# Kernel optimization log

Measured on AMD Instinct MI355X. Metric: run time of the kernel, lower is better.

The kernel has to match this reference:

```python
import jax, jax.numpy as jnp
import numpy as np

B, T1, O, E, H = 32, 65, 384, 384, 768  # T1 = T+1


def setup_inputs() -> dict:
    key = jax.random.key(0)
    ks = jax.random.split(key, 10)
    s = 0.05
    return {
        "target": jax.random.randint(ks[0], (B, T1), 0, O),
        "hidden": jax.random.normal(ks[1], (B, H), jnp.float32),
        "teacher_forcing_ratio": 1,
        "emb_table": jax.random.normal(ks[2], (O, E), jnp.float32) * s,
        "attn_W": jax.random.normal(ks[3], (H, H + O), jnp.float32) * s,
        "attn_b": jnp.zeros((H,), jnp.float32),
        "v_W": jax.random.normal(ks[4], (1, H), jnp.float32) * s,
        "gru_Wih": jax.random.normal(ks[5], (3 * H, E + O), jnp.float32) * s,
        "gru_Whh": jax.random.normal(ks[6], (3 * H, H), jnp.float32) * s,
        "gru_bih": jnp.zeros((3 * H,), jnp.float32),
        "gru_bhh": jnp.zeros((3 * H,), jnp.float32),
        "fc_W": jax.random.normal(ks[7], (O, E + O + H), jnp.float32) * s,
        "fc_b": jnp.zeros((O,), jnp.float32),
    }


def reference(target, hidden, teacher_forcing_ratio, emb_table, attn_W, attn_b,
              v_W, gru_Wih, gru_Whh, gru_bih, gru_bhh, fc_W, fc_b):
    # teacher_forcing_ratio == 1: always teacher-forced (deterministic)
    Bt, T1_ = target.shape
    T = T1_ - 1
    Od = fc_b.shape[0]
    Hd = hidden.shape[1]
    pos = jnp.arange(T1_)
    hist0 = jnp.zeros((Bt, T1_, Od), hidden.dtype)  # slot 0 = initial zeros output

    def step(carry, xs):
        h, hist = carry
        i, tok = xs
        emb = emb_table[tok]  # (B, E)
        # Bahdanau attention over history positions 0..i
        hrep = jnp.broadcast_to(h[:, None, :], (Bt, T1_, Hd))
        energy = jnp.tanh(jnp.concatenate([hrep, hist], -1) @ attn_W.T + attn_b)
        scores = jnp.squeeze(energy @ v_W.T, -1)  # (B, T1)
        scores = jnp.where(pos <= i, scores, -jnp.inf)
        a = jax.nn.softmax(scores, axis=-1)
        w = jnp.einsum('bt,bto->bo', a, hist)  # context (B, O)
        # single-step GRU (PyTorch gate order r, z, n)
        x = jnp.concatenate([emb, w], -1)
        gi = x @ gru_Wih.T + gru_bih
        gh = h @ gru_Whh.T + gru_bhh
        ir, iz, inn = jnp.split(gi, 3, axis=-1)
        hr, hz, hn = jnp.split(gh, 3, axis=-1)
        r = jax.nn.sigmoid(ir + hr)
        z = jax.nn.sigmoid(iz + hz)
        n = jnp.tanh(inn + r * hn)
        h_new = (1.0 - z) * n + z * h
        out = jnp.concatenate([h_new, w, emb], -1) @ fc_W.T + fc_b  # (B, O)
        hist = hist.at[:, i + 1].set(out)
        return (h_new, hist), (out, a)

    xs = (jnp.arange(T), target[:, :T].T)  # input token at step i is target[:, i]
    _, (outs, attns) = jax.lax.scan(step, (hidden, hist0), xs)
    outputs = jnp.transpose(outs, (1, 2, 0))  # (B, O, T)
    # flatten per-step attentions: step i has i+1 valid entries -> T*(T+1)/2 total
    rows = np.concatenate([np.full(i + 1, i) for i in range(T)])
    cols = np.concatenate([np.arange(i + 1) for i in range(T)])
    attentions = attns[rows, :, cols].T  # (B, T*(T+1)/2)
    return outputs, attentions
```

## Files before the change

kernel.cpp:

```cpp
#include <hip/hip_runtime.h>


#define DEVI static __device__ __forceinline__
typedef float f32x4 __attribute__((ext_vector_type(4)));
typedef unsigned u32x4 __attribute__((ext_vector_type(4)));
typedef unsigned u32x2 __attribute__((ext_vector_type(2)));
typedef unsigned short ushort_t;

constexpr int ATTN_OFF = 786432;

constexpr int OFF_HALL  = 0;
constexpr int OFF_U     = 1597440;
constexpr int OFF_WALL  = 1622016;
constexpr int OFF_HISTF = 2408448;
constexpr int OFF_GH    = 3194880;
constexpr int OFF_GIE   = 3268608;
constexpr int OFF_FE    = 3342336;
constexpr int OFF_GE    = 3354624;
constexpr int OFF_FP    = 3379200;
constexpr int OFF_CP    = 3391488;
constexpr int OFF_GHM   = 3416064;
constexpr int OFF_GWM   = 4005888;
constexpr int OFF_GEM   = 4300800;
constexpr int OFF_GB    = 4595712;
constexpr int OFF_V1    = 4596480;
constexpr int OFF_BAR   = 4596512;
constexpr int OFF_F32END= 4597664;
constexpr int O16_CALL = 0;
constexpr int O16_HIST = 1572864;

DEVI float fast_tanh(float x) {
  float a = __builtin_fabsf(x);
  float e = __expf(-2.0f * a);
  float r = __fdividef(1.0f - e, 1.0f + e);
  return __builtin_copysignf(r, x);
}
DEVI float sigmoidf_(float x) { return __fdividef(1.0f, 1.0f + __expf(-x)); }
DEVI float bflo(unsigned u) { return __uint_as_float(u << 16); }
DEVI float bfhi(unsigned u) { return __uint_as_float(u & 0xffff0000u); }
DEVI unsigned f2bf(float f) {
  unsigned u = __float_as_uint(f);
  return (u + 0x7fffu + ((u >> 16) & 1u)) >> 16;
}

DEVI float nc_ld_f1(const float* p) {
  float r;
  asm volatile("global_load_dword %0, %1, off sc0 sc1\n\ts_waitcnt vmcnt(0)"
               : "=&v"(r) : "v"(p) : "memory");
  return r;
}
DEVI f32x4 nc_ld4(const float* p) {
  f32x4 r;
  asm volatile("global_load_dwordx4 %0, %1, off sc0 sc1\n\ts_waitcnt vmcnt(0)"
               : "=&v"(r) : "v"(p) : "memory");
  return r;
}
DEVI void nc_ld4x2(const float* p0, const float* p1, f32x4& r0, f32x4& r1) {
  asm volatile(
      "global_load_dwordx4 %0, %2, off sc0 sc1\n\t"
      "global_load_dwordx4 %1, %3, off sc0 sc1\n\t"
      "s_waitcnt vmcnt(0)"
      : "=&v"(r0), "=&v"(r1) : "v"(p0), "v"(p1) : "memory");
}
DEVI void nc_st4(float* p, f32x4 v) {
  asm volatile("global_store_dwordx4 %0, %1, off sc0 sc1" :: "v"(p), "v"(v) : "memory");
}
DEVI void nc_st2u(ushort_t* p, u32x2 v) {
  asm volatile("global_store_dwordx2 %0, %1, off sc0 sc1" :: "v"(p), "v"(v) : "memory");
}
DEVI void nc_st_f1(float* p, float v_) {
  asm volatile("global_store_dword %0, %1, off sc0 sc1" :: "v"(p), "v"(v_) : "memory");
}

DEVI void gridbar(unsigned* bar) {
  asm volatile("s_waitcnt vmcnt(0)" ::: "memory");
  __syncthreads();
  if (threadIdx.x == 0) {
    unsigned* super = bar + 1024;
    unsigned* gen   = bar + 1056;
    unsigned g = __hip_atomic_load(gen, __ATOMIC_RELAXED, __HIP_MEMORY_SCOPE_AGENT);
    int grp = (int)(blockIdx.x >> 3);
    unsigned a = __hip_atomic_fetch_add(bar + grp * 32, 1u, __ATOMIC_RELAXED, __HIP_MEMORY_SCOPE_AGENT);
    bool released = false;
    if (a == 7u) {
      __hip_atomic_store(bar + grp * 32, 0u, __ATOMIC_RELAXED, __HIP_MEMORY_SCOPE_AGENT);
      unsigned s = __hip_atomic_fetch_add(super, 1u, __ATOMIC_RELAXED, __HIP_MEMORY_SCOPE_AGENT);
      if (s == 31u) {
        __hip_atomic_store(super, 0u, __ATOMIC_RELAXED, __HIP_MEMORY_SCOPE_AGENT);
        __hip_atomic_fetch_add(gen, 1u, __ATOMIC_RELAXED, __HIP_MEMORY_SCOPE_AGENT);
        released = true;
      }
    }
    if (!released) {
      while (__hip_atomic_load(gen, __ATOMIC_RELAXED, __HIP_MEMORY_SCOPE_AGENT) == g) {
        __builtin_amdgcn_s_sleep(1);
      }
    }
  }
  __syncthreads();
}

__global__ __launch_bounds__(256) void kprepG(const float* __restrict__ attn_W,
                                              const float* __restrict__ fcW,
                                              const float* __restrict__ fcb,
                                              float* __restrict__ ws) {
  int bid = blockIdx.x, tid = threadIdx.x;
  if (bid < 288) {
    int rt = bid / 6, kt = bid % 6;
    int r0 = rt * 16;
    int kg = kt * 256 + tid;
    float acc[16];
#pragma unroll
    for (int q = 0; q < 16; ++q) acc[q] = 0.f;
    for (int o = 0; o < 384; ++o) {
      float f = fcW[o * 1536 + kg];
#pragma unroll
      for (int q = 0; q < 16; ++q)
        acc[q] = fmaf(attn_W[(r0 + q) * 1152 + 768 + o], f, acc[q]);
    }
#pragma unroll
    for (int q = 0; q < 16; ++q) {
      int r = r0 + q;
      if (kg < 768)       ws[OFF_GHM + r * 768 + kg] = acc[q];
      else if (kg < 1152) ws[OFF_GWM + r * 384 + (kg - 768)] = acc[q];
      else                ws[OFF_GEM + r * 384 + (kg - 1152)] = acc[q];
    }
  } else {
    for (int r = tid; r < 768; r += 256) {
      float a = 0.f;
      for (int o = 0; o < 384; ++o) a = fmaf(attn_W[r * 1152 + 768 + o], fcb[o], a);
      ws[OFF_GB + r] = a;
    }
  }
}

__global__ __launch_bounds__(256) void kprep0(const float* __restrict__ hidden,
                                              const float* __restrict__ vW,
                                              float* __restrict__ ws) {
  ushort_t* w16 = (ushort_t*)(ws + OFF_F32END);
  int bid = blockIdx.x, tid = threadIdx.x;
  int gtid = bid * 256 + tid;
  if (gtid < 24576) {
    int k = gtid >> 5, b = gtid & 31;
    ws[OFF_HALL + gtid] = hidden[b * 768 + k];
  } else if (gtid < 36864) {
    ((unsigned*)(w16 + O16_CALL))[gtid - 24576] = 0u;
  } else if (gtid < 43008) {
    ((unsigned*)(w16 + O16_HIST))[gtid - 36864] = 0u;
  }
  if (gtid < 1152) ((unsigned*)(ws + OFF_BAR))[gtid] = 0u;
  if (bid == 0) {
    __shared__ float vred[256];
    float a = 0.f;
    for (int k = tid; k < 768; k += 256) a += __builtin_fabsf(vW[k]);
    vred[tid] = a;
    __syncthreads();
    for (int s2 = 128; s2 > 0; s2 >>= 1) {
      if (tid < s2) vred[tid] += vred[tid + s2];
      __syncthreads();
    }
    if (tid == 0) ws[OFF_V1] = vred[0];
  }
}

__global__ void __launch_bounds__(1024)
kmain(const int* __restrict__ target, const float* __restrict__ emb,
      const float* __restrict__ attn_W, const float* __restrict__ attn_b,
      const float* __restrict__ vW,
      const float* __restrict__ Wih, const float* __restrict__ Whh,
      const float* __restrict__ bih, const float* __restrict__ bhh,
      const float* __restrict__ fcW, const float* __restrict__ fcb,
      float* __restrict__ outp, float* __restrict__ ws) {
  const int bid = blockIdx.x, tid = threadIdx.x;
  const int wv = tid >> 6, lane = tid & 63;
  const int b32 = lane & 31, kh = lane >> 5;
  const int vb = ((bid & 7) << 5) | (bid >> 3);
  const int xcd = vb >> 5, slot = vb & 31;
  unsigned* bar = (unsigned*)(ws + OFF_BAR);
  ushort_t* w16 = (ushort_t*)(ws + OFF_F32END);

  __shared__ __align__(16) float sW_A[8 * 768];
  __shared__ __align__(16) float sW_B[16 * 384];
  __shared__ __align__(16) float sW_GH[12 * 768];
  __shared__ __align__(16) float sW_C[14 * 384];
  __shared__ __align__(16) float sUn[13536];

  const int gbA = (vb * 480) >> 8, geA = ((vb + 1) * 480) >> 8;
  const int rbA = gbA * 4;
  const int nswA = geA - gbA;
  const int nRA = nswA * 4;
  const int lb  = xcd * 28 + (slot - 4);
  const int rbB = (slot >= 4) ? (lb * 3456) / 224 : 0;
  const int reB = (slot >= 4) ? ((lb + 1) * 3456) / 224 : 0;
  const int nB  = reB - rbB;
  const int gbG = (slot >= 4) ? (lb * 576) / 224 : 0;
  const int geG = (slot >= 4) ? ((lb + 1) * 576) / 224 : 0;
  const int nswG = geG - gbG;
  const int nRG = nswG * 4;
  const int rbC = xcd * 144 + ((slot * 144) >> 5);
  const int reC = xcd * 144 + (((slot + 1) * 144) >> 5);

  for (int lr = 0; lr < nRA; ++lr) {
    int row = rbA + lr;
    const float* src;
    if (row < 768)       src = attn_W + row * 1152;
    else if (row < 1536) src = ws + OFF_GHM + (row - 768) * 768;
    else                 src = fcW + (row - 1536) * 1536;
    if (tid < 768) sW_A[lr * 768 + tid] = src[tid];
  }
  if (slot >= 4) {
    for (int lr = 0; lr < nB; ++lr) {
      int row = rbB + lr;
      const float* src;
      if (row < 2304)      src = Wih + row * 768;
      else if (row < 2688) src = fcW + (row - 2304) * 1536 + 1152;
      else                 src = ws + OFF_GEM + (row - 2688) * 384;
      if (tid < 384) sW_B[lr * 384 + tid] = src[tid];
    }
    for (int lr = 0; lr < nRG; ++lr) {
      int row = gbG * 4 + lr;
      if (tid < 768) sW_GH[lr * 768 + tid] = Whh[row * 768 + tid];
    }
  }
  for (int lr = 0; lr < 14; ++lr) {
    const float* src = nullptr;
    if (lr < 9) {
      int grow = vb * 3 + (lr / 3) + (lr % 3) * 768;
      src = Wih + grow * 768 + 384;
    } else {
      int r = rbC + (lr - 9);
      if (r < reC) src = (r < 384) ? fcW + r * 1536 + 768
                                   : ws + OFF_GWM + (r - 384) * 384;
    }
    if (src && tid < 384) sW_C[lr * 384 + tid] = src[tid];
  }
  __syncthreads();

  const float Mv = ws[OFF_V1];
  const int k0 = wv * 48 + kh * 24;

  for (int i = 0; i < 64; ++i) {
    {
      float* part_  = sUn;
      float* stage  = sUn + 4096;
      float* stage2 = sUn + 4352;
      float xr[24];
      const float* hb = ws + OFF_HALL + i * 24576 + b32;
#pragma unroll
      for (int q = 0; q < 24; ++q) xr[q] = hb[(k0 + q) * 32];

      float a[8];
#pragma unroll
      for (int r = 0; r < 8; ++r) a[r] = 0.f;
#pragma unroll
      for (int r = 0; r < 8; ++r) {
        if (r < nRA) {
          int row = rbA + r;
          if (!(i == 0 && row >= 768)) {
            const float* wp = &sW_A[r * 768 + k0];
            float acc = 0.f;
#pragma unroll
            for (int q = 0; q < 6; ++q) {
              f32x4 w = *(const f32x4*)(wp + q * 4);
              acc = fmaf(w[0], xr[q * 4 + 0], acc);
              acc = fmaf(w[1], xr[q * 4 + 1], acc);
              acc = fmaf(w[2], xr[q * 4 + 2], acc);
              acc = fmaf(w[3], xr[q * 4 + 3], acc);
            }
            a[r] = acc;
          }
        }
      }
#pragma unroll
      for (int r = 0; r < 8; ++r) a[r] += __shfl_xor(a[r], 32);
      if (kh == 0) {
#pragma unroll
        for (int r = 0; r < 8; ++r) part_[wv * 256 + r * 32 + b32] = a[r];
      }
      __syncthreads();
      if (tid < 256) {
        int rr = tid >> 5, bb = tid & 31;
        float sum = 0.f;
#pragma unroll
        for (int w2 = 0; w2 < 16; ++w2) sum += part_[w2 * 256 + tid];
        if (rr < nRA) {
          int row = rbA + rr;
          if (row < 768) sum += attn_b[row];
          stage[rr * 32 + bb] = sum;
        }
      } else if (tid < 320) {
        int t2 = tid - 256, rr = t2 >> 3, bq = t2 & 7;
        if (rr < nRA && i > 0) {
          int row = rbA + rr;
          if (row >= 768) {
            const float* src = row < 1536
                ? ws + OFF_CP + (row - 768) * 32 + bq * 4
                : ws + OFF_FP + (row - 1536) * 32 + bq * 4;
            *(f32x4*)&stage2[rr * 32 + bq * 4] = nc_ld4(src);
          }
        }
      }
      __syncthreads();
      if (tid < 64) {
        int gsel = tid >> 5, sub = tid & 31;
        if (gsel < nswA) {
          int row0 = rbA + gsel * 4;
          int e0 = gsel * 4;
          if (row0 < 768) {
            f32x4 v = {stage[e0 * 32 + sub], stage[(e0 + 1) * 32 + sub],
                       stage[(e0 + 2) * 32 + sub], stage[(e0 + 3) * 32 + sub]};
            nc_st4(ws + OFF_U + sub * 768 + row0, v);
          } else if (i > 0) {
            float v0 = stage[e0 * 32 + sub] + stage2[e0 * 32 + sub];
            float v1 = stage[(e0 + 1) * 32 + sub] + stage2[(e0 + 1) * 32 + sub];
            float v2 = stage[(e0 + 2) * 32 + sub] + stage2[(e0 + 2) * 32 + sub];
            float v3 = stage[(e0 + 3) * 32 + sub] + stage2[(e0 + 3) * 32 + sub];
            u32x2 pk;
            pk[0] = f2bf(v0) | (f2bf(v1) << 16);
            pk[1] = f2bf(v2) | (f2bf(v3) << 16);
            if (row0 < 1536) {
              nc_st2u(w16 + O16_CALL + i * 24576 + sub * 768 + (row0 - 768), pk);
            } else {
              nc_st2u(w16 + O16_HIST + i * 12288 + sub * 384 + (row0 - 1536), pk);
              f32x4 vf = {v0, v1, v2, v3};
              nc_st4(ws + OFF_HISTF + i * 12288 + sub * 384 + (row0 - 1536), vf);
            }
          }
        }
      }
    }
    gridbar(bar);

    if (slot < 4) {
      const int bb = xcd * 4 + (vb & 3);
      float* u_s   = sUn;
      float* p_l   = sUn + 768;
      float* d_l   = sUn + 832;
      float* wred2 = sUn + 848;
      if (tid < 192) *(f32x4*)&u_s[tid * 4] = nc_ld4(ws + OFF_U + bb * 768 + tid * 4);
      if (tid < 64) p_l[tid] = 0.f;
      __syncthreads();
      const int tl = tid >> 5, kc = tid & 31;
      float u_r[24], v_r[24];
#pragma unroll
      for (int q = 0; q < 24; ++q) {
        u_r[q] = u_s[kc * 24 + q];
        v_r[q] = vW[kc * 24 + q];
      }
#pragma unroll
      for (int rr2 = 0; rr2 < 2; ++rr2) {
        int t = rr2 * 32 + tl;
        float s = 0.f;
        if (t <= i) {
          const ushort_t* cb = w16 + O16_CALL + t * 24576 + bb * 768 + kc * 24;
          u32x4 c0 = ((const u32x4*)cb)[0];
          u32x4 c1 = ((const u32x4*)cb)[1];
          u32x4 c2 = ((const u32x4*)cb)[2];
#pragma unroll
          for (int j = 0; j < 4; ++j) {
            s = fmaf(fast_tanh(u_r[2 * j] + bflo(c0[j])), v_r[2 * j], s);
            s = fmaf(fast_tanh(u_r[2 * j + 1] + bfhi(c0[j])), v_r[2 * j + 1], s);
            s = fmaf(fast_tanh(u_r[8 + 2 * j] + bflo(c1[j])), v_r[8 + 2 * j], s);
            s = fmaf(fast_tanh(u_r[8 + 2 * j + 1] + bfhi(c1[j])), v_r[8 + 2 * j + 1], s);
            s = fmaf(fast_tanh(u_r[16 + 2 * j] + bflo(c2[j])), v_r[16 + 2 * j], s);
            s = fmaf(fast_tanh(u_r[16 + 2 * j + 1] + bfhi(c2[j])), v_r[16 + 2 * j + 1], s);
          }
        }
#pragma unroll
        for (int d2 = 16; d2 >= 1; d2 >>= 1) s += __shfl_xor(s, d2);
        if (kc == 0 && t <= i) p_l[t] = __expf(s - Mv);
      }
      __syncthreads();
      if (tid < 64) {
        float pv = p_l[tid];
#pragma unroll
        for (int d = 1; d < 64; d <<= 1) pv += __shfl_xor(pv, d);
        if (tid == 0) d_l[0] = __fdividef(1.0f, pv);
      }
      __syncthreads();
      float dinv = d_l[0];
      if (tid >= 768 && tid < 832) {
        int t = tid - 768;
        if (t <= i)
          outp[ATTN_OFF + bb * 2080 + (i * (i + 1)) / 2 + t] = p_l[t] * dinv;
      }
      if (tid < 768) {
        int opair = tid % 192, tpar = tid / 192;
        int o0 = opair * 2;
        const ushort_t* hbase = w16 + O16_HIST + bb * 384 + o0;
        float a0 = 0.f, a1 = 0.f;
        int t = tpar;
        for (; t + 4 <= i; t += 8) {
          unsigned hv0 = *(const unsigned*)(hbase + t * 12288);
          unsigned hv1 = *(const unsigned*)(hbase + (t + 4) * 12288);
          float p0 = p_l[t], p1 = p_l[t + 4];
          a0 = fmaf(p0, bflo(hv0), a0);
          a1 = fmaf(p0, bfhi(hv0), a1);
          a0 = fmaf(p1, bflo(hv1), a0);
          a1 = fmaf(p1, bfhi(hv1), a1);
        }
        if (t <= i) {
          unsigned hv = *(const unsigned*)(hbase + t * 12288);
          float p = p_l[t];
          a0 = fmaf(p, bflo(hv), a0);
          a1 = fmaf(p, bfhi(hv), a1);
        }
        wred2[tpar * 384 + o0]     = a0;
        wred2[tpar * 384 + o0 + 1] = a1;
      }
      __syncthreads();
      if (tid < 96) {
        f32x4 v;
#pragma unroll
        for (int e = 0; e < 4; ++e) {
          int o = tid * 4 + e;
          v[e] = (wred2[o] + wred2[384 + o] + wred2[768 + o] + wred2[1152 + o]) * dinv;
        }
        nc_st4(ws + OFF_WALL + i * 12288 + bb * 384 + tid * 4, v);
      }
    } else {
      float* part_  = sUn;
      float* stageB = sUn + 2048;
      float* ghst   = sUn + 8192;
      const int gl = wv >> 2, kq = wv & 3;
      const int tok = target[b32 * 65 + i];
      const int koff = kq * 96 + kh * 48;
      const float* xe = emb + tok * 384 + koff;
      f32x4 x_[12];
#pragma unroll
      for (int q = 0; q < 12; ++q) x_[q] = *(const f32x4*)(xe + q * 4);
      float a[4];
#pragma unroll
      for (int r = 0; r < 4; ++r) {
        int lr = gl * 4 + r;
        float acc = 0.f;
        if (lr < nB) {
          const float* wp = &sW_B[lr * 384 + koff];
#pragma unroll
          for (int q = 0; q < 12; ++q) {
            f32x4 w = *(const f32x4*)(wp + q * 4);
            acc = fmaf(w[0], x_[q][0], acc);
            acc = fmaf(w[1], x_[q][1], acc);
            acc = fmaf(w[2], x_[q][2], acc);
            acc = fmaf(w[3], x_[q][3], acc);
          }
        }
        a[r] = acc;
      }
#pragma unroll
      for (int r = 0; r < 4; ++r) a[r] += __shfl_xor(a[r], 32);
      if (kh == 0) {
#pragma unroll
        for (int r = 0; r < 4; ++r)
          part_[((gl * 4 + r) * 4 + kq) * 32 + b32] = a[r];
      }
      __syncthreads();
      if (tid < 512) {
        int glr = tid >> 5, bb = tid & 31;
        if (glr < nB) {
          float sum = part_[(glr * 4 + 0) * 32 + bb] + part_[(glr * 4 + 1) * 32 + bb]
                    + part_[(glr * 4 + 2) * 32 + bb] + part_[(glr * 4 + 3) * 32 + bb];
          int row = rbB + glr;
          if (row < 2304) sum += bih[row];
          else if (row < 2688) sum += fcb[row - 2304];
          else sum += ws[OFF_GB + (row - 2688)];
          stageB[glr * 32 + bb] = sum;
        }
      }
      __syncthreads();
      if (tid < 128) {
        int r16 = tid >> 3, bq = tid & 7;
        if (r16 < nB) {
          int row = rbB + r16;
          f32x4 v = *(f32x4*)&stageB[r16 * 32 + bq * 4];
          float* dst;
          if (row < 2304) dst = ws + OFF_GIE + row * 32 + bq * 4;
          else if (row < 2688) dst = ws + OFF_FE + (row - 2304) * 32 + bq * 4;
          else dst = ws + OFF_GE + (row - 2688) * 32 + bq * 4;
          nc_st4(dst, v);
        }
      }
      __syncthreads();
      {
        float xr2[24];
        const float* hb2 = ws + OFF_HALL + i * 24576 + b32;
#pragma unroll
        for (int q = 0; q < 24; ++q) xr2[q] = hb2[(k0 + q) * 32];
        float a2[12];
#pragma unroll
        for (int r = 0; r < 12; ++r) a2[r] = 0.f;
#pragma unroll
        for (int r = 0; r < 12; ++r) {
          if (r < nRG) {
            const float* wp = &sW_GH[r * 768 + k0];
            float acc = 0.f;
#pragma unroll
            for (int q = 0; q < 6; ++q) {
              f32x4 w = *(const f32x4*)(wp + q * 4);
              acc = fmaf(w[0], xr2[q * 4 + 0], acc);
              acc = fmaf(w[1], xr2[q * 4 + 1], acc);
              acc = fmaf(w[2], xr2[q * 4 + 2], acc);
              acc = fmaf(w[3], xr2[q * 4 + 3], acc);
            }
            a2[r] = acc;
          }
        }
#pragma unroll
        for (int r = 0; r < 12; ++r) a2[r] += __shfl_xor(a2[r], 32);
        if (kh == 0) {
#pragma unroll
          for (int r = 0; r < 12; ++r) part_[wv * 384 + r * 32 + b32] = a2[r];
        }
        __syncthreads();
        if (tid < 384) {
          int rr = tid >> 5, bb = tid & 31;
          if (rr < nRG) {
            float sum = 0.f;
#pragma unroll
            for (int w2 = 0; w2 < 16; ++w2) sum += part_[w2 * 384 + tid];
            ghst[rr * 32 + bb] = sum + bhh[gbG * 4 + rr];
          }
        }
        __syncthreads();
        if (tid < 96) {
          int rr = tid >> 3, bq = tid & 7;
          if (rr < nRG)
            nc_st4(ws + OFF_GH + (gbG * 4 + rr) * 32 + bq * 4,
                   *(f32x4*)&ghst[rr * 32 + bq * 4]);
        }
      }
    }
    gridbar(bar);

    {
      float* w_lds   = sUn;
      float* g_lds   = sUn + 12416;
      float* giw_lds = sUn + 12992;
      float* fpst    = sUn + 13280;
      float* gat     = sUn + 13440;
      {
        int b = tid >> 5, c = tid & 31;
        const float* src = ws + OFF_WALL + i * 12288 + tid * 12;
        float* dst = w_lds + b * 388 + c * 12;
        *(f32x4*)&dst[0] = *(const f32x4*)(src);
        *(f32x4*)&dst[4] = *(const f32x4*)(src + 4);
        *(f32x4*)&dst[8] = *(const f32x4*)(src + 8);
      }
      __syncthreads();
      if (wv < 9) {
        int jl = wv / 3, gg = wv % 3;
        const float* wp = &sW_C[(jl * 3 + gg) * 384 + kh * 192];
        const float* xp = w_lds + b32 * 388 + kh * 192;
        float acc = 0.f;
#pragma unroll 8
        for (int q = 0; q < 48; ++q) {
          f32x4 wq4 = *(const f32x4*)(wp + q * 4);
          f32x4 xq4 = *(const f32x4*)(xp + q * 4);
          acc = fmaf(wq4[0], xq4[0], acc); acc = fmaf(wq4[1], xq4[1], acc);
          acc = fmaf(wq4[2], xq4[2], acc); acc = fmaf(wq4[3], xq4[3], acc);
        }
        acc += __shfl_xor(acc, 32);
        if (kh == 0) giw_lds[(jl * 3 + gg) * 32 + b32] = acc;
      } else if (wv < 14) {
        int r = rbC + (wv - 9);
        if (r < reC) {
          const float* wp = &sW_C[(9 + (wv - 9)) * 384 + kh * 192];
          const float* xp = w_lds + b32 * 388 + kh * 192;
          float acc = 0.f;
#pragma unroll 8
          for (int q = 0; q < 48; ++q) {
            f32x4 wq4 = *(const f32x4*)(wp + q * 4);
            f32x4 xq4 = *(const f32x4*)(xp + q * 4);
            acc = fmaf(wq4[0], xq4[0], acc); acc = fmaf(wq4[1], xq4[1], acc);
            acc = fmaf(wq4[2], xq4[2], acc); acc = fmaf(wq4[3], xq4[3], acc);
          }
          acc += __shfl_xor(acc, 32);
          if (kh == 0) fpst[(wv - 9) * 32 + b32] = acc;
        }
      } else {
        int t2 = tid - 896;
        if (t2 < 72) {
          int q0 = 2 * t2, q1 = 2 * t2 + 1;
          const float* pa;
          const float* pb;
          {
            int row = q0 >> 3, bq = q0 & 7;
            int rr2 = row < 9 ? row : row - 9;
            int r = vb * 3 + (rr2 % 3) + (rr2 / 3) * 768;
            pa = ws + (row < 9 ? OFF_GIE : OFF_GH) + r * 32 + bq * 4;
          }
          {
            int row = q1 >> 3, bq = q1 & 7;
            int rr2 = row < 9 ? row : row - 9;
            int r = vb * 3 + (rr2 % 3) + (rr2 / 3) * 768;
            pb = ws + (row < 9 ? OFF_GIE : OFF_GH) + r * 32 + bq * 4;
          }
          f32x4 v0, v1;
          nc_ld4x2(pa, pb, v0, v1);
          *(f32x4*)&g_lds[q0 * 4] = v0;
          *(f32x4*)&g_lds[q1 * 4] = v1;
        }
      }
      __syncthreads();
      if (tid < 96) {
        int jl = tid >> 5, bb = tid & 31;
        int j = vb * 3 + jl;
        float gi_r = g_lds[jl * 32 + bb];
        float gi_z = g_lds[(3 + jl) * 32 + bb];
        float gi_n = g_lds[(6 + jl) * 32 + bb];
        float gh_r = g_lds[(9 + jl) * 32 + bb];
        float gh_z = g_lds[(12 + jl) * 32 + bb];
        float gh_n = g_lds[(15 + jl) * 32 + bb];
        float giw_r = giw_lds[(jl * 3 + 0) * 32 + bb];
        float giw_z = giw_lds[(jl * 3 + 1) * 32 + bb];
        float giw_n = giw_lds[(jl * 3 + 2) * 32 + bb];
        float hold = ws[OFF_HALL + i * 24576 + j * 32 + bb];
        float r_ = sigmoidf_(gi_r + giw_r + gh_r);
        float z_ = sigmoidf_(gi_z + giw_z + gh_z);
        float n_ = fast_tanh(fmaf(r_, gh_n, gi_n + giw_n));
        gat[jl * 32 + bb] = (1.0f - z_) * n_ + z_ * hold;
      } else if (tid >= 96 && tid < 136) {
        int t2 = tid - 96, rl = t2 >> 3, bq = t2 & 7;
        int r = rbC + rl;
        if (r < reC) {
          const float* addp = r < 384 ? ws + OFF_FE + r * 32 + bq * 4
                                      : ws + OFF_GE + (r - 384) * 32 + bq * 4;
          f32x4 ad = nc_ld4(addp);
          f32x4 v;
#pragma unroll
          for (int e = 0; e < 4; ++e) v[e] = fpst[rl * 32 + bq * 4 + e] + ad[e];
          float* dst = r < 384 ? ws + OFF_FP + r * 32 + bq * 4
                               : ws + OFF_CP + (r - 384) * 32 + bq * 4;
          nc_st4(dst, v);
        }
      }
      __syncthreads();
      if (tid < 24) {
        int jl3 = tid >> 3, bq = tid & 7;
        f32x4 v = *(f32x4*)&gat[jl3 * 32 + bq * 4];
        nc_st4(ws + OFF_HALL + (i + 1) * 24576 + (vb * 3 + jl3) * 32 + bq * 4, v);
      }
    }
    gridbar(bar);
  }

  if (slot < 3) {
    int o = xcd * 48 + slot * 16 + wv;
    const float* hcol = ws + OFF_HALL + 64 * 24576 + b32;
    const float* wrow = fcW + o * 1536 + kh * 384;
    float acc = 0.f;
#pragma unroll 4
    for (int q = 0; q < 96; ++q) {
      f32x4 wq = *(const f32x4*)(wrow + q * 4);
      int k = kh * 384 + q * 4;
      acc = fmaf(wq[0], hcol[k * 32], acc);
      acc = fmaf(wq[1], hcol[(k + 1) * 32], acc);
      acc = fmaf(wq[2], hcol[(k + 2) * 32], acc);
      acc = fmaf(wq[3], hcol[(k + 3) * 32], acc);
    }
    acc += __shfl_xor(acc, 32);
    if (kh == 0) {
      float fp = nc_ld_f1(ws + OFF_FP + o * 32 + b32);
      outp[b32 * 24576 + o * 64 + 63] = acc + fp;
    }
  }
  if (tid < 48) {
    int pair = vb * 48 + tid;
    int b = pair / 384, o = pair - b * 384;
    const float* src = ws + OFF_HISTF + b * 384 + o;
    float* dst = outp + b * 24576 + o * 64;
#pragma unroll 7
    for (int t = 0; t < 63; ++t) dst[t] = src[(t + 1) * 12288];
  }
}

extern "C" void kernel_launch(void* const* d_in, const int* in_sizes, int n_in,
                              void* d_out, int out_size, void* d_ws, size_t ws_size,
                              hipStream_t stream) {
  const int*   target = (const int*)d_in[0];
  const float* hidden = (const float*)d_in[1];
  const float* emb    = (const float*)d_in[3];
  const float* attn_W = (const float*)d_in[4];
  const float* attn_b = (const float*)d_in[5];
  const float* vW     = (const float*)d_in[6];
  const float* Wih    = (const float*)d_in[7];
  const float* Whh    = (const float*)d_in[8];
  const float* bih    = (const float*)d_in[9];
  const float* bhh    = (const float*)d_in[10];
  const float* fcW    = (const float*)d_in[11];
  const float* fcb    = (const float*)d_in[12];
  float* outp = (float*)d_out;
  float* ws   = (float*)d_ws;

  kprepG<<<289, 256, 0, stream>>>(attn_W, fcW, fcb, ws);
  kprep0<<<256, 256, 0, stream>>>(hidden, vW, ws);

  void* args[] = {(void*)&target, (void*)&emb, (void*)&attn_W, (void*)&attn_b,
                  (void*)&vW, (void*)&Wih, (void*)&Whh, (void*)&bih, (void*)&bhh,
                  (void*)&fcW, (void*)&fcb, (void*)&outp, (void*)&ws};
  hipLaunchCooperativeKernel((const void*)kmain, dim3(256), dim3(1024), args, 0, stream);
}
```

Measured before the change: 1.859 ms.

## Split grid barrier into arrive/wait with monotonic counters, skipping wait for non-attention blocks

Replaces the reset-based grid barrier with a split arrive/wait barrier. It uses four rotating slots of monotonically increasing group, super and release counters, which removes the counter reset stores. After the first phase, only blocks that consume its results (slot < 4) wait. The other blocks proceed straight into their independent work, overlapping the barrier latency. This adds more barrier state and relies on those blocks truly not reading the first-phase outputs.

```diff
diff --git a/kernel.cpp b/kernel.cpp
--- a/kernel.cpp
+++ b/kernel.cpp
@@ -25,7 +25,7 @@
 constexpr int OFF_GB    = 4595712;
 constexpr int OFF_V1    = 4596480;
 constexpr int OFF_BAR   = 4596512;
-constexpr int OFF_F32END= 4597664;
+constexpr int OFF_F32END= 4598688;
 constexpr int O16_CALL = 0;
 constexpr int O16_HIST = 1572864;
 
@@ -72,30 +72,25 @@
   asm volatile("global_store_dword %0, %1, off sc0 sc1" :: "v"(p), "v"(v_) : "memory");
 }
 
-DEVI void gridbar(unsigned* bar) {
+DEVI void bar_arrive(unsigned* bar, unsigned bk) {
   asm volatile("s_waitcnt vmcnt(0)" ::: "memory");
   __syncthreads();
   if (threadIdx.x == 0) {
-    unsigned* super = bar + 1024;
-    unsigned* gen   = bar + 1056;
-    unsigned g = __hip_atomic_load(gen, __ATOMIC_RELAXED, __HIP_MEMORY_SCOPE_AGENT);
-    int grp = (int)(blockIdx.x >> 3);
-    unsigned a = __hip_atomic_fetch_add(bar + grp * 32, 1u, __ATOMIC_RELAXED, __HIP_MEMORY_SCOPE_AGENT);
-    bool released = false;
-    if (a == 7u) {
-      __hip_atomic_store(bar + grp * 32, 0u, __ATOMIC_RELAXED, __HIP_MEMORY_SCOPE_AGENT);
-      unsigned s = __hip_atomic_fetch_add(super, 1u, __ATOMIC_RELAXED, __HIP_MEMORY_SCOPE_AGENT);
-      if (s == 31u) {
-        __hip_atomic_store(super, 0u, __ATOMIC_RELAXED, __HIP_MEMORY_SCOPE_AGENT);
-        __hip_atomic_fetch_add(gen, 1u, __ATOMIC_RELAXED, __HIP_MEMORY_SCOPE_AGENT);
-        released = true;
-      }
-    }
-    if (!released) {
-      while (__hip_atomic_load(gen, __ATOMIC_RELAXED, __HIP_MEMORY_SCOPE_AGENT) == g) {
-        __builtin_amdgcn_s_sleep(1);
-      }
-    }
+    unsigned s = bk & 3u, u = bk >> 2;
+    unsigned* grpc = bar + s * 512 + ((blockIdx.x >> 3) << 4);
+    unsigned a = __hip_atomic_fetch_add(grpc, 1u, __ATOMIC_RELAXED, __HIP_MEMORY_SCOPE_AGENT);
+    if (a == 8u * u + 7u) {
+      unsigned t = __hip_atomic_fetch_add(bar + 2048 + s * 16, 1u, __ATOMIC_RELAXED, __HIP_MEMORY_SCOPE_AGENT);
+      if (t == 32u * u + 31u)
+        __hip_atomic_fetch_add(bar + 2112 + s * 16, 1u, __ATOMIC_RELAXED, __HIP_MEMORY_SCOPE_AGENT);
+    }
+  }
+}
+DEVI void bar_wait(unsigned* bar, unsigned bk) {
+  if (threadIdx.x == 0) {
+    unsigned s = bk & 3u, u = bk >> 2;
+    while (__hip_atomic_load(bar + 2112 + s * 16, __ATOMIC_RELAXED, __HIP_MEMORY_SCOPE_AGENT) < u + 1u)
+      __builtin_amdgcn_s_sleep(1);
   }
   __syncthreads();
 }
@@ -148,7 +143,7 @@
   } else if (gtid < 43008) {
     ((unsigned*)(w16 + O16_HIST))[gtid - 36864] = 0u;
   }
-  if (gtid < 1152) ((unsigned*)(ws + OFF_BAR))[gtid] = 0u;
+  if (gtid < 2176) ((unsigned*)(ws + OFF_BAR))[gtid] = 0u;
   if (bid == 0) {
     __shared__ float vred[256];
     float a = 0.f;
@@ -238,6 +233,7 @@
 
   const float Mv = ws[OFF_V1];
   const int k0 = wv * 48 + kh * 24;
+  unsigned bk = 0;
 
   for (int i = 0; i < 64; ++i) {
     {
@@ -329,9 +325,10 @@
         }
       }
     }
-    gridbar(bar);
+    bar_arrive(bar, bk);
 
     if (slot < 4) {
+      bar_wait(bar, bk);
       const int bb = xcd * 4 + (vb & 3);
       float* u_s   = sUn;
       float* p_l   = sUn + 768;
@@ -530,7 +527,10 @@
         }
       }
     }
-    gridbar(bar);
+    ++bk;
+    bar_arrive(bar, bk);
+    bar_wait(bar, bk);
+    ++bk;
 
     {
       float* w_lds   = sUn;
@@ -641,7 +641,9 @@
         nc_st4(ws + OFF_HALL + (i + 1) * 24576 + (vb * 3 + jl3) * 32 + bq * 4, v);
       }
     }
-    gridbar(bar);
+    bar_arrive(bar, bk);
+    bar_wait(bar, bk);
+    ++bk;
   }
 
   if (slot < 3) {
```

Result: faster. 1.763 ms, median of 2 (-5.2%).
